# Optimization experiments

Hardware: AMD Instinct MI355X
Metric: run time of the kernel (lower is better)

## Reference

```python
import jax, jax.numpy as jnp
import numpy as np
import math

D_MODEL = 1024
N_HEAD = 16
HEAD_DIM = D_MODEL // N_HEAD
BATCH = 4
MAX_LEN = 1024


def _shift(BD):
    # BD: (b, h, L, 2L) -> (b, h, L, L), Transformer-XL relative shift
    b, h, L, _ = BD.shape
    zero_pad = jnp.zeros((b, h, L, 1), BD.dtype)
    BD = jnp.concatenate([BD, zero_pad], axis=-1)      # (b,h,L,2L+1)
    BD = BD.reshape(b, h, -1, L)[:, :, :-1]            # (b,h,2L,L)
    BD = BD.reshape(b, h, L, -1)                       # (b,h,L,2L)
    return BD[:, :, :, L:]                             # (b,h,L,L)


def setup_inputs() -> dict:
    key = jax.random.key(0)
    ks = jax.random.split(key, 10)
    s = 1.0 / math.sqrt(D_MODEL)
    return {
        "q": jax.random.normal(ks[0], (BATCH, MAX_LEN, D_MODEL), jnp.float32),
        "k": jax.random.normal(ks[1], (BATCH, MAX_LEN, D_MODEL), jnp.float32),
        "mask": jax.random.randint(ks[2], (BATCH, MAX_LEN), 0, 2, jnp.int32),
        "pos_embed": jax.random.normal(ks[3], (2 * MAX_LEN, HEAD_DIM), jnp.float32),
        "Wq": jax.random.normal(ks[4], (D_MODEL, D_MODEL), jnp.float32) * s,
        "Wkv": jax.random.normal(ks[5], (D_MODEL, 2 * D_MODEL), jnp.float32) * s,
        "Wr": jax.random.normal(ks[6], (HEAD_DIM, HEAD_DIM), jnp.float32) / math.sqrt(HEAD_DIM),
        "r_r_bias": jax.random.normal(ks[7], (N_HEAD, HEAD_DIM), jnp.float32) * 0.02,
        "r_w_bias": jax.random.normal(ks[8], (N_HEAD, HEAD_DIM), jnp.float32) * 0.02,
    }


def reference(q, k, mask, pos_embed, Wq, Wkv, Wr, r_r_bias, r_w_bias):
    B, L, D = q.shape
    H = r_r_bias.shape[0]
    hd = D // H
    scale = math.sqrt(hd)

    r = pos_embed @ Wr                                   # (2L, hd)
    qh = (q @ Wq).reshape(B, L, H, hd).transpose(0, 2, 1, 3)   # (B,H,L,hd)
    kv = k @ Wkv                                         # (B,L,2D)
    kk, vv = jnp.split(kv, 2, axis=-1)
    kh = kk.reshape(B, L, H, hd).transpose(0, 2, 1, 3)
    vh = vv.reshape(B, L, H, hd).transpose(0, 2, 1, 3)

    AC = jnp.einsum('bhqd,bhkd->bhqk', qh + r_r_bias[None, :, None, :], kh)
    BD = jnp.einsum('bhqd,ld->bhql', qh + r_w_bias[None, :, None, :], r)  # (B,H,L,2L)
    BD = _shift(BD)

    attn = (AC + BD) / scale
    attn = jnp.where(mask[:, None, None, :] == 0, -jnp.inf, attn)
    attn = jax.nn.softmax(attn, axis=-1)

    out = jnp.einsum('bhqk,bhkd->bhqd', attn, vh)        # (B,H,L,hd)
    return out.transpose(0, 2, 1, 3).reshape(B, L, D)
```

## Files before the change

kernel.cpp:

```cpp
#include <hip/hip_runtime.h>

typedef short bf16x8 __attribute__((ext_vector_type(8)));
typedef float f32x4 __attribute__((ext_vector_type(4)));
typedef unsigned short u16;
typedef unsigned short u16x4 __attribute__((ext_vector_type(4)));
typedef unsigned short u16x8 __attribute__((ext_vector_type(8)));
typedef unsigned int u32;

#define NB 4
#define LEN 1024
#define DM 1024
#define NH 16
#define HD 64

#define QSCALE 0.18033688011112043f

__device__ __forceinline__ u16 f2bf(float f) {
    union { float f; unsigned u; } v; v.f = f;
    return (u16)((v.u + 0x7fffu + ((v.u >> 16) & 1u)) >> 16);
}

__device__ __forceinline__ float bf2f(u16 x) {
    union { float f; unsigned u; } v; v.u = ((unsigned)x) << 16;
    return v.f;
}

__device__ __forceinline__ float exp2f_fast(float x) {
    float r; asm("v_exp_f32 %0, %1" : "=v"(r) : "v"(x)); return r;
}

__device__ __forceinline__ unsigned cvt_pk_bf16(float a, float b) {
    unsigned r; asm("v_cvt_pk_bf16_f32 %0, %1, %2" : "=v"(r) : "v"(a), "v"(b)); return r;
}

__device__ __forceinline__ f32x4 mfma16(bf16x8 a, bf16x8 b, f32x4 c) {
    return __builtin_amdgcn_mfma_f32_16x16x32_bf16(a, b, c, 0, 0, 0);
}

__device__ __forceinline__ void gload16(const void* g, void* l) {
    __builtin_amdgcn_global_load_lds(
        (const __attribute__((address_space(1))) unsigned int*)g,
        (__attribute__((address_space(3))) unsigned int*)l, 16, 0, 0);
}

__global__ void prep(const float* __restrict__ q, const float* __restrict__ k,
                     const int* __restrict__ msk,
                     const float* __restrict__ Wq, const float* __restrict__ Wkv,
                     const float* __restrict__ pos, const float* __restrict__ Wr,
                     u16* __restrict__ qbf, u16* __restrict__ kbf,
                     u16* __restrict__ WqT, u16* __restrict__ WkvT,
                     u16* __restrict__ rbf, float* __restrict__ mb) {
    __shared__ float tile[32][33];
    const int f = blockIdx.x;
    const int tid = threadIdx.x;
    if (f < 3072) {
        const int x = f % 96, y = f / 96;
        const bool isQ = x < 32;
        const float* W = isQ ? Wq : Wkv;
        u16* WT = isQ ? WqT : WkvT;
        const int N = isQ ? 1024 : 2048;
        const int n0 = (isQ ? x : x - 32) * 32;
        const int k0 = y * 32;
        const int tx = tid & 31, ty = tid >> 5;
        #pragma unroll
        for (int j = 0; j < 4; j++) {
            int r = ty + j * 8;
            tile[r][tx] = W[(size_t)(k0 + r) * N + n0 + tx];
        }
        __syncthreads();
        #pragma unroll
        for (int j = 0; j < 4; j++) {
            int r = ty + j * 8;
            WT[(size_t)(n0 + r) * 1024 + k0 + tx] = f2bf(tile[tx][r]);
        }
    } else if (f < 3588) {
        int idx = (f - 3072) * 256 + tid;
        if (idx < 2064 * 64) {
            int row = idx >> 6, col = idx & 63;
            float s = 0.f;
            if (row < 2048) {
                #pragma unroll
                for (int kk = 0; kk < 64; kk++) s += pos[row * 64 + kk] * Wr[kk * 64 + col];
            }
            const int csw = (((col >> 3) ^ (row & 7)) << 3) | (col & 7);
            rbf[(row << 6) | csw] = f2bf(s);
        }
    } else if (f < 3604) {
        int i = (f - 3588) * 256 + tid;
        if (i < NB * LEN) mb[i] = msk[i] ? 0.f : -3.0e38f;
    } else {
        int idx = (f - 3604) * 256 + tid;
        if (idx < 1048576) {
            float4 v = ((const float4*)q)[idx];
            u16x4 o;
            o[0] = f2bf(v.x); o[1] = f2bf(v.y); o[2] = f2bf(v.z); o[3] = f2bf(v.w);
            ((u16x4*)qbf)[idx] = o;
        } else if (idx < 2097152) {
            int i = idx - 1048576;
            float4 v = ((const float4*)k)[i];
            u16x4 o;
            o[0] = f2bf(v.x); o[1] = f2bf(v.y); o[2] = f2bf(v.z); o[3] = f2bf(v.w);
            ((u16x4*)kbf)[i] = o;
        }
    }
}

__global__ __launch_bounds__(256) void gemm_all(
    const u16* __restrict__ qbf, const u16* __restrict__ kbf,
    const u16* __restrict__ WqT, const u16* __restrict__ WkvT,
    const float* __restrict__ rrb,
    u16* __restrict__ A1,
    u16* __restrict__ khs, u16* __restrict__ vhsT)
{
    __shared__ u16 as[2][128][32];
    __shared__ u16 bs[2][128][32];

    const int fb = blockIdx.x;
    const int wsw = ((fb & 7) * 96) + (fb >> 3);
    const int bx = wsw % 24;
    const bool isQ = bx < 8;
    const u16* Abf = isQ ? qbf : kbf;
    const u16* BT  = isQ ? WqT : WkvT;
    const int n0 = (isQ ? bx : bx - 8) * 128;
    const int m0 = (wsw / 24) * 128;
    const int tid = threadIdx.x;
    const int w = tid >> 6, lane = tid & 63, g = lane >> 4, c = lane & 15;
    const int wm = w >> 1, wn = w & 1;
    const int srow = lane >> 2, sj = lane & 3;

    const f32x4 fzero = {0.f, 0.f, 0.f, 0.f};
    f32x4 acc[4][4];
    #pragma unroll
    for (int i = 0; i < 4; i++)
        #pragma unroll
        for (int j = 0; j < 4; j++) acc[i][j] = fzero;

    auto STAGE = [&](int buf, int ks) {
        const int k0 = ks * 32;
        #pragma unroll
        for (int i = 0; i < 2; i++) {
            const int rb = w * 32 + i * 16;
            const int rowA = rb + srow;
            gload16(Abf + (size_t)(m0 + rowA) * 1024 + k0 + ((sj ^ (rowA & 3)) << 3),
                    &as[buf][rb][0]);
            gload16(BT + (size_t)(n0 + rowA) * 1024 + k0 + ((sj ^ (rowA & 3)) << 3),
                    &bs[buf][rb][0]);
        }
    };

    STAGE(0, 0);
    __syncthreads();

    for (int ks = 0; ks < 32; ks++) {
        const int cur = ks & 1, nb = cur ^ 1;
        if (ks < 31) STAGE(nb, ks + 1);

        bf16x8 af[4], bfr[4];
        #pragma unroll
        for (int i = 0; i < 4; i++) {
            const int row = wm * 64 + i * 16 + c;
            af[i] = *(const bf16x8*)&as[cur][row][(g ^ (row & 3)) << 3];
        }
        #pragma unroll
        for (int j = 0; j < 4; j++) {
            const int row = wn * 64 + j * 16 + c;
            bfr[j] = *(const bf16x8*)&bs[cur][row][(g ^ (row & 3)) << 3];
        }
        #pragma unroll
        for (int i = 0; i < 4; i++)
            #pragma unroll
            for (int j = 0; j < 4; j++)
                acc[i][j] = mfma16(af[i], bfr[j], acc[i][j]);

        __syncthreads();
    }

    #pragma unroll
    for (int j = 0; j < 4; j++) {
        const int n = n0 + wn * 64 + j * 16 + c;
        float b1v = 0.f;
        if (isQ) b1v = rrb[n];
        #pragma unroll
        for (int i = 0; i < 4; i++) {
            const int l0 = m0 + wm * 64 + i * 16 + 4 * g;
            if (!isQ && n >= DM) {
                const int d = n & 63, hh = (n - DM) >> 6;
                const int bb = l0 >> 10, l = l0 & 1023;
                u16x4 o;
                #pragma unroll
                for (int r = 0; r < 4; r++) o[r] = f2bf(acc[i][j][r]);
                *(u16x4*)(vhsT + (((size_t)(bb * NH + hh)) * HD + d) * LEN + l) = o;
            } else {
                #pragma unroll
                for (int r = 0; r < 4; r++) {
                    const int row = l0 + r;
                    const int bb = row >> 10, l = row & 1023;
                    const float v = acc[i][j][r];
                    if (isQ) {
                        size_t idx = (((size_t)(bb * NH + (n >> 6))) * LEN + l) * HD + (n & 63);
                        A1[idx] = f2bf((v + b1v) * QSCALE);
                    } else {
                        const int d = n & 63;
                        const int dsw = (((d >> 3) ^ (l & 7)) << 3) | (d & 7);
                        size_t idx = (((size_t)(bb * NH + (n >> 6))) * LEN + l) * HD + dsw;
                        khs[idx] = f2bf(v);
                    }
                }
            }
        }
    }
}

__global__ __launch_bounds__(512, 4) void attn_kernel(
    const u16* __restrict__ A1,
    const u16* __restrict__ khs, const u16* __restrict__ vhsT,
    const u16* __restrict__ rbf, const float* __restrict__ mbias,
    const float* __restrict__ rrb, const float* __restrict__ rwb,
    float* __restrict__ outp)
{
    __shared__ u16 kbuf[2][32][64];
    __shared__ u16 rbuf[224][64];
    __shared__ u16 vbuf[2][4][64][8];
    __shared__ float biasl[1024];
    __shared__ float gl[8][16][52];

    const int bh = blockIdx.x;
    const int b = bh >> 4, h = bh & 15;
    const int tid = threadIdx.x;
    const int w = tid >> 6, lane = tid & 63, g = lane >> 4, c = lane & 15;
    const int q0 = blockIdx.y * 128, q0w = q0 + w * 16;
    const int lrow8 = lane >> 3, lcol = lane & 7;
    const int kkey = (c + 1) & 7;

    const u16* Kbase = khs + (size_t)bh * LEN * HD;
    const u16* Vp = vhsT + (size_t)bh * HD * LEN;
    float* glw = &gl[w][0][0];
    u16* pw = (u16*)glw;

    const u16* A1p = A1 + ((size_t)bh * LEN + q0w) * HD;
    bf16x8 a1f[2], a2f[2];
    #pragma unroll
    for (int kf = 0; kf < 2; kf++)
        a1f[kf] = *(const bf16x8*)(A1p + c * HD + kf * 32 + g * 8);
    {
        const float* rrbp = rrb + h * HD;
        const float* rwbp = rwb + h * HD;
        #pragma unroll
        for (int kf = 0; kf < 2; kf++) {
            const int dbase = kf * 32 + g * 8;
            f32x4 rA0 = *(const f32x4*)(rrbp + dbase);
            f32x4 rA1 = *(const f32x4*)(rrbp + dbase + 4);
            f32x4 rB0 = *(const f32x4*)(rwbp + dbase);
            f32x4 rB1 = *(const f32x4*)(rwbp + dbase + 4);
            float a2v[8];
            #pragma unroll
            for (int e = 0; e < 4; e++) {
                a2v[e]     = bf2f((u16)a1f[kf][e])     + (rB0[e] - rA0[e]) * QSCALE;
                a2v[4 + e] = bf2f((u16)a1f[kf][4 + e]) + (rB1[e] - rA1[e]) * QSCALE;
            }
            union { u32 u[4]; bf16x8 v; } cv;
            cv.u[0] = cvt_pk_bf16(a2v[0], a2v[1]);
            cv.u[1] = cvt_pk_bf16(a2v[2], a2v[3]);
            cv.u[2] = cvt_pk_bf16(a2v[4], a2v[5]);
            cv.u[3] = cvt_pk_bf16(a2v[6], a2v[7]);
            a2f[kf] = cv.v;
        }
    }

    const int js0 = LEN - q0 - 128;
    if (w < 4) {
        gload16(Kbase + (((size_t)(8 * w + lrow8)) << 6) + (lcol << 3), &kbuf[0][8 * w][0]);
        gload16(Vp + ((size_t)lane << 10) + 8 * w, &vbuf[0][w][0][0]);
    } else {
        gload16(mbias + b * LEN + (w - 4) * 256 + lane * 4, &biasl[(w - 4) * 256]);
    }
    #pragma unroll
    for (int i = 0; i < 3; i++) {
        const int row = js0 + 8 * (w + 8 * i);
        gload16(rbf + (((size_t)(row + lrow8)) << 6) + (lcol << 3), &rbuf[row % 224][0]);
    }
    __syncthreads();

    bf16x8 RA[2], RB[2];
    int bs = (1009 - q0w) % 224;
    {
        int t = bs + c; if (t >= 224) t -= 224;
        #pragma unroll
        for (int kf = 0; kf < 2; kf++)
            RA[kf] = *(const bf16x8*)&rbuf[t][((4 * kf + g) ^ kkey) * 8];
    }

    const f32x4 fzero = {0.f, 0.f, 0.f, 0.f};
    f32x4 oacc[4];
    #pragma unroll
    for (int dt = 0; dt < 4; dt++) oacc[dt] = fzero;
    float mrow = -3.0e38f, lrow = 0.f;

    auto STEP = [&](int kt, bf16x8 (&Rold)[2], bf16x8 (&Rnew)[2]) {
        const int cur = kt & 1, nb = cur ^ 1;
        const int c0 = kt * 32;

        if (w < 4) {
            if (kt < 31) {
                const int c0n = c0 + 32;
                gload16(Kbase + (((size_t)(c0n + 8 * w + lrow8)) << 6) + (lcol << 3), &kbuf[nb][8 * w][0]);
                gload16(Vp + ((size_t)lane << 10) + c0n + 8 * w, &vbuf[nb][w][0][0]);
            }
        } else {
            if (kt < 30) {
                const int row0 = js0 + 192 + 32 * kt + 8 * (w - 4);
                gload16(rbf + (((size_t)(row0 + lrow8)) << 6) + (lcol << 3), &rbuf[row0 % 224][0]);
            }
        }

        bf16x8 Kf[2][2];
        #pragma unroll
        for (int ct = 0; ct < 2; ct++)
            #pragma unroll
            for (int kf = 0; kf < 2; kf++)
                Kf[ct][kf] = *(const bf16x8*)&kbuf[cur][16 * ct + c][((4 * kf + g) ^ (c & 7)) * 8];

        bf16x8 Rf1[2], Rf2[2];
        {
            int t = bs + 16 + c; if (t >= 224) t -= 224;
            #pragma unroll
            for (int kf = 0; kf < 2; kf++)
                Rf1[kf] = *(const bf16x8*)&rbuf[t][((4 * kf + g) ^ kkey) * 8];
        }
        {
            int t = bs + 32 + c; if (t >= 224) t -= 224;
            #pragma unroll
            for (int kf = 0; kf < 2; kf++) {
                Rf2[kf] = *(const bf16x8*)&rbuf[t][((4 * kf + g) ^ kkey) * 8];
                Rnew[kf] = Rf2[kf];
            }
        }

        __builtin_amdgcn_s_setprio(1);
        f32x4 s0 = fzero, s1 = fzero;
        s0 = mfma16(Kf[0][0], a1f[0], s0);
        s0 = mfma16(Kf[0][1], a1f[1], s0);
        s1 = mfma16(Kf[1][0], a1f[0], s1);
        s1 = mfma16(Kf[1][1], a1f[1], s1);
        f32x4 g0 = fzero, g1 = fzero, g2 = fzero;
        g0 = mfma16(Rold[0], a2f[0], g0);
        g0 = mfma16(Rold[1], a2f[1], g0);
        *(f32x4*)&glw[c * 52 + 4 * g] = g0;
        g1 = mfma16(Rf1[0], a2f[0], g1);
        g1 = mfma16(Rf1[1], a2f[1], g1);
        *(f32x4*)&glw[c * 52 + 16 + 4 * g] = g1;
        g2 = mfma16(Rf2[0], a2f[0], g2);
        g2 = mfma16(Rf2[1], a2f[1], g2);
        *(f32x4*)&glw[c * 52 + 32 + 4 * g] = g2;
        __builtin_amdgcn_s_setprio(0);

        const float* glq = &glw[c * 52];
        f32x4 bb0 = *(const f32x4*)&biasl[c0 + 4 * g];
        f32x4 bb1 = *(const f32x4*)&biasl[c0 + 16 + 4 * g];
        #pragma unroll
        for (int r = 0; r < 4; r++) {
            const int gidx = 4 * g + r + 15 - c;
            s0[r] += glq[gidx] + bb0[r];
            s1[r] += glq[gidx + 16] + bb1[r];
        }

        float t = fmaxf(fmaxf(fmaxf(s0[0], s0[1]), fmaxf(s0[2], s0[3])),
                        fmaxf(fmaxf(s1[0], s1[1]), fmaxf(s1[2], s1[3])));
        t = fmaxf(t, __shfl_xor(t, 16));
        t = fmaxf(t, __shfl_xor(t, 32));
        if (!__all(t <= mrow + 8.f)) {
            const float mnew = fmaxf(mrow, t);
            const float alpha = exp2f_fast(mrow - mnew);
            mrow = mnew;
            lrow *= alpha;
            #pragma unroll
            for (int dt = 0; dt < 4; dt++)
                #pragma unroll
                for (int r = 0; r < 4; r++) oacc[dt][r] *= alpha;
        }
        float p[8];
        float ps = 0.f;
        #pragma unroll
        for (int r = 0; r < 4; r++) {
            p[r] = exp2f_fast(s0[r] - mrow);
            p[4 + r] = exp2f_fast(s1[r] - mrow);
            ps += p[r] + p[4 + r];
        }
        lrow += ps;
        const unsigned d0 = cvt_pk_bf16(p[0], p[1]);
        const unsigned d1 = cvt_pk_bf16(p[2], p[3]);
        const unsigned d2 = cvt_pk_bf16(p[4], p[5]);
        const unsigned d3 = cvt_pk_bf16(p[6], p[7]);
        *(uint2*)&pw[c * 104 + 4 * g] = make_uint2(d0, d1);
        *(uint2*)&pw[c * 104 + 16 + 4 * g] = make_uint2(d2, d3);
        bf16x8 pbr = *(const bf16x8*)&pw[c * 104 + 8 * g];

        bf16x8 Vb[4];
        #pragma unroll
        for (int dt = 0; dt < 4; dt++)
            Vb[dt] = *(const bf16x8*)&vbuf[cur][g][16 * dt + c][0];
        __builtin_amdgcn_s_setprio(1);
        #pragma unroll
        for (int dt = 0; dt < 4; dt++)
            oacc[dt] = mfma16(Vb[dt], pbr, oacc[dt]);
        __builtin_amdgcn_s_setprio(0);

        bs += 32; if (bs >= 224) bs -= 224;
        __syncthreads();
    };

    for (int kt2 = 0; kt2 < 16; kt2++) {
        STEP(2 * kt2,     RA, RB);
        STEP(2 * kt2 + 1, RB, RA);
    }

    float sum = lrow;
    sum += __shfl_xor(sum, 16);
    sum += __shfl_xor(sum, 32);
    const float inv = sum > 0.f ? 1.0f / sum : 0.f;
    const int l = q0w + c;
    float* op = outp + ((size_t)b * LEN + l) * DM + h * HD;
    #pragma unroll
    for (int dt = 0; dt < 4; dt++) {
        f32x4 o;
        #pragma unroll
        for (int r = 0; r < 4; r++) o[r] = oacc[dt][r] * inv;
        *(f32x4*)(op + dt * 16 + 4 * g) = o;
    }
}

extern "C" void kernel_launch(void* const* d_in, const int* in_sizes, int n_in,
                              void* d_out, int out_size, void* d_ws, size_t ws_size,
                              hipStream_t stream) {
    const float* q   = (const float*)d_in[0];
    const float* k   = (const float*)d_in[1];
    const int*   msk = (const int*)d_in[2];
    const float* pos = (const float*)d_in[3];
    const float* Wq  = (const float*)d_in[4];
    const float* Wkv = (const float*)d_in[5];
    const float* Wr  = (const float*)d_in[6];
    const float* rrb = (const float*)d_in[7];
    const float* rwb = (const float*)d_in[8];
    float* outp = (float*)d_out;
    char* ws = (char*)d_ws;

    u16* qbf  = (u16*)(ws + 0);
    u16* kbf  = (u16*)(ws + 8388608);
    u16* WqT  = (u16*)(ws + 16777216);
    u16* WkvT = (u16*)(ws + 18874368);
    u16* rbf  = (u16*)(ws + 23068672);
    u16* A1   = (u16*)(ws + 23332864);
    u16* khs  = (u16*)(ws + 40110080);
    u16* vhsT = (u16*)(ws + 48498688);
    float* mb = (float*)(ws + 56887296);

    prep<<<11796, 256, 0, stream>>>(q, k, msk, Wq, Wkv, pos, Wr, qbf, kbf, WqT, WkvT, rbf, mb);
    gemm_all<<<768, 256, 0, stream>>>(qbf, kbf, WqT, WkvT, rrb, A1, khs, vhsT);
    attn_kernel<<<dim3(64, 8), 512, 0, stream>>>(A1, khs, vhsT, rbf, mb, rrb, rwb, outp);
}
```

Before: 113.6 us.

## Fuse fp32-to-bf16 activation conversion into GEMM A-tile staging

The separate pass that converted q and k from fp32 to bf16 in a workspace is removed. The GEMM now loads fp32 A tiles into registers, converts them with packed bf16 conversions, and writes them to swizzled LDS, overlapping the load with the MFMA loop. The small pos@Wr and mask-bias jobs move from the prep kernel into extra blocks of the GEMM launch. This saves a full read-write round trip of the activations, at the cost of twice the A-tile global traffic in the GEMM, more register pressure, and one conversion per k-step per GEMM block, repeated across the 24 N tiles.

```diff
diff --git a/kernel.cpp b/kernel.cpp
--- a/kernel.cpp
+++ b/kernel.cpp
@@ -6,6 +6,7 @@
 typedef unsigned short u16x4 __attribute__((ext_vector_type(4)));
 typedef unsigned short u16x8 __attribute__((ext_vector_type(8)));
 typedef unsigned int u32;
+typedef unsigned int u32x4 __attribute__((ext_vector_type(4)));
 
 #define NB 4
 #define LEN 1024
@@ -43,90 +44,79 @@
         (__attribute__((address_space(3))) unsigned int*)l, 16, 0, 0);
 }
 
-__global__ void prep(const float* __restrict__ q, const float* __restrict__ k,
-                     const int* __restrict__ msk,
-                     const float* __restrict__ Wq, const float* __restrict__ Wkv,
-                     const float* __restrict__ pos, const float* __restrict__ Wr,
-                     u16* __restrict__ qbf, u16* __restrict__ kbf,
-                     u16* __restrict__ WqT, u16* __restrict__ WkvT,
-                     u16* __restrict__ rbf, float* __restrict__ mb) {
+__global__ void prep(const float* __restrict__ Wq, const float* __restrict__ Wkv,
+                     u16* __restrict__ WqT, u16* __restrict__ WkvT) {
     __shared__ float tile[32][33];
     const int f = blockIdx.x;
     const int tid = threadIdx.x;
-    if (f < 3072) {
-        const int x = f % 96, y = f / 96;
-        const bool isQ = x < 32;
-        const float* W = isQ ? Wq : Wkv;
-        u16* WT = isQ ? WqT : WkvT;
-        const int N = isQ ? 1024 : 2048;
-        const int n0 = (isQ ? x : x - 32) * 32;
-        const int k0 = y * 32;
-        const int tx = tid & 31, ty = tid >> 5;
-        #pragma unroll
-        for (int j = 0; j < 4; j++) {
-            int r = ty + j * 8;
-            tile[r][tx] = W[(size_t)(k0 + r) * N + n0 + tx];
-        }
-        __syncthreads();
-        #pragma unroll
-        for (int j = 0; j < 4; j++) {
-            int r = ty + j * 8;
-            WT[(size_t)(n0 + r) * 1024 + k0 + tx] = f2bf(tile[tx][r]);
-        }
-    } else if (f < 3588) {
-        int idx = (f - 3072) * 256 + tid;
-        if (idx < 2064 * 64) {
-            int row = idx >> 6, col = idx & 63;
-            float s = 0.f;
-            if (row < 2048) {
-                #pragma unroll
-                for (int kk = 0; kk < 64; kk++) s += pos[row * 64 + kk] * Wr[kk * 64 + col];
-            }
-            const int csw = (((col >> 3) ^ (row & 7)) << 3) | (col & 7);
-            rbf[(row << 6) | csw] = f2bf(s);
-        }
-    } else if (f < 3604) {
-        int i = (f - 3588) * 256 + tid;
-        if (i < NB * LEN) mb[i] = msk[i] ? 0.f : -3.0e38f;
-    } else {
-        int idx = (f - 3604) * 256 + tid;
-        if (idx < 1048576) {
-            float4 v = ((const float4*)q)[idx];
-            u16x4 o;
-            o[0] = f2bf(v.x); o[1] = f2bf(v.y); o[2] = f2bf(v.z); o[3] = f2bf(v.w);
-            ((u16x4*)qbf)[idx] = o;
-        } else if (idx < 2097152) {
-            int i = idx - 1048576;
-            float4 v = ((const float4*)k)[i];
-            u16x4 o;
-            o[0] = f2bf(v.x); o[1] = f2bf(v.y); o[2] = f2bf(v.z); o[3] = f2bf(v.w);
-            ((u16x4*)kbf)[i] = o;
-        }
+    const int x = f % 96, y = f / 96;
+    const bool isQ = x < 32;
+    const float* W = isQ ? Wq : Wkv;
+    u16* WT = isQ ? WqT : WkvT;
+    const int N = isQ ? 1024 : 2048;
+    const int n0 = (isQ ? x : x - 32) * 32;
+    const int k0 = y * 32;
+    const int tx = tid & 31, ty = tid >> 5;
+    #pragma unroll
+    for (int j = 0; j < 4; j++) {
+        int r = ty + j * 8;
+        tile[r][tx] = W[(size_t)(k0 + r) * N + n0 + tx];
+    }
+    __syncthreads();
+    #pragma unroll
+    for (int j = 0; j < 4; j++) {
+        int r = ty + j * 8;
+        WT[(size_t)(n0 + r) * 1024 + k0 + tx] = f2bf(tile[tx][r]);
     }
 }
 
 __global__ __launch_bounds__(256) void gemm_all(
-    const u16* __restrict__ qbf, const u16* __restrict__ kbf,
+    const float* __restrict__ qf, const float* __restrict__ kf32,
     const u16* __restrict__ WqT, const u16* __restrict__ WkvT,
     const float* __restrict__ rrb,
+    const float* __restrict__ pos, const float* __restrict__ Wr,
+    const int* __restrict__ msk,
     u16* __restrict__ A1,
-    u16* __restrict__ khs, u16* __restrict__ vhsT)
+    u16* __restrict__ khs, u16* __restrict__ vhsT,
+    u16* __restrict__ rbf, float* __restrict__ mb)
 {
     __shared__ u16 as[2][128][32];
     __shared__ u16 bs[2][128][32];
 
     const int fb = blockIdx.x;
+    const int tid = threadIdx.x;
+
+    if (fb >= 768) {
+        if (fb < 1284) {
+            int idx = (fb - 768) * 256 + tid;
+            if (idx < 2064 * 64) {
+                int row = idx >> 6, col = idx & 63;
+                float s = 0.f;
+                if (row < 2048) {
+                    #pragma unroll
+                    for (int kk = 0; kk < 64; kk++) s += pos[row * 64 + kk] * Wr[kk * 64 + col];
+                }
+                const int csw = (((col >> 3) ^ (row & 7)) << 3) | (col & 7);
+                rbf[(row << 6) | csw] = f2bf(s);
+            }
+        } else {
+            int i = (fb - 1284) * 256 + tid;
+            if (i < NB * LEN) mb[i] = msk[i] ? 0.f : -3.0e38f;
+        }
+        return;
+    }
+
     const int wsw = ((fb & 7) * 96) + (fb >> 3);
     const int bx = wsw % 24;
     const bool isQ = bx < 8;
-    const u16* Abf = isQ ? qbf : kbf;
+    const float* Af = isQ ? qf : kf32;
     const u16* BT  = isQ ? WqT : WkvT;
     const int n0 = (isQ ? bx : bx - 8) * 128;
     const int m0 = (wsw / 24) * 128;
-    const int tid = threadIdx.x;
     const int w = tid >> 6, lane = tid & 63, g = lane >> 4, c = lane & 15;
     const int wm = w >> 1, wn = w & 1;
     const int srow = lane >> 2, sj = lane & 3;
+    const int arow = tid >> 1, ahalf = tid & 1;
 
     const f32x4 fzero = {0.f, 0.f, 0.f, 0.f};
     f32x4 acc[4][4];
@@ -135,25 +125,40 @@
         #pragma unroll
         for (int j = 0; j < 4; j++) acc[i][j] = fzero;
 
-    auto STAGE = [&](int buf, int ks) {
+    float4 fa[4];
+    const float* Abase = Af + (size_t)(m0 + arow) * 1024 + ahalf * 16;
+
+    auto STAGE_LOAD = [&](int ks, int buf) {
         const int k0 = ks * 32;
+        const float4* Ap = (const float4*)(Abase + k0);
+        fa[0] = Ap[0]; fa[1] = Ap[1]; fa[2] = Ap[2]; fa[3] = Ap[3];
         #pragma unroll
         for (int i = 0; i < 2; i++) {
             const int rb = w * 32 + i * 16;
-            const int rowA = rb + srow;
-            gload16(Abf + (size_t)(m0 + rowA) * 1024 + k0 + ((sj ^ (rowA & 3)) << 3),
-                    &as[buf][rb][0]);
-            gload16(BT + (size_t)(n0 + rowA) * 1024 + k0 + ((sj ^ (rowA & 3)) << 3),
+            const int rowB = rb + srow;
+            gload16(BT + (size_t)(n0 + rowB) * 1024 + k0 + ((sj ^ (rowB & 3)) << 3),
                     &bs[buf][rb][0]);
         }
     };
 
-    STAGE(0, 0);
+    auto STAGE_WRITE = [&](int buf) {
+        u32x4 d0, d1;
+        d0[0] = cvt_pk_bf16(fa[0].x, fa[0].y); d0[1] = cvt_pk_bf16(fa[0].z, fa[0].w);
+        d0[2] = cvt_pk_bf16(fa[1].x, fa[1].y); d0[3] = cvt_pk_bf16(fa[1].z, fa[1].w);
+        d1[0] = cvt_pk_bf16(fa[2].x, fa[2].y); d1[1] = cvt_pk_bf16(fa[2].z, fa[2].w);
+        d1[2] = cvt_pk_bf16(fa[3].x, fa[3].y); d1[3] = cvt_pk_bf16(fa[3].z, fa[3].w);
+        const int j0 = 2 * ahalf, j1 = j0 + 1;
+        *(u32x4*)&as[buf][arow][((j0 ^ (arow & 3)) << 3)] = d0;
+        *(u32x4*)&as[buf][arow][((j1 ^ (arow & 3)) << 3)] = d1;
+    };
+
+    STAGE_LOAD(0, 0);
+    STAGE_WRITE(0);
     __syncthreads();
 
     for (int ks = 0; ks < 32; ks++) {
         const int cur = ks & 1, nb = cur ^ 1;
-        if (ks < 31) STAGE(nb, ks + 1);
+        if (ks < 31) STAGE_LOAD(ks + 1, nb);
 
         bf16x8 af[4], bfr[4];
         #pragma unroll
@@ -172,6 +177,7 @@
             for (int j = 0; j < 4; j++)
                 acc[i][j] = mfma16(af[i], bfr[j], acc[i][j]);
 
+        if (ks < 31) STAGE_WRITE(nb);
         __syncthreads();
     }
 
@@ -444,8 +450,6 @@
     float* outp = (float*)d_out;
     char* ws = (char*)d_ws;
 
-    u16* qbf  = (u16*)(ws + 0);
-    u16* kbf  = (u16*)(ws + 8388608);
     u16* WqT  = (u16*)(ws + 16777216);
     u16* WkvT = (u16*)(ws + 18874368);
     u16* rbf  = (u16*)(ws + 23068672);
@@ -454,7 +458,8 @@
     u16* vhsT = (u16*)(ws + 48498688);
     float* mb = (float*)(ws + 56887296);
 
-    prep<<<11796, 256, 0, stream>>>(q, k, msk, Wq, Wkv, pos, Wr, qbf, kbf, WqT, WkvT, rbf, mb);
-    gemm_all<<<768, 256, 0, stream>>>(qbf, kbf, WqT, WkvT, rrb, A1, khs, vhsT);
+    prep<<<3072, 256, 0, stream>>>(Wq, Wkv, WqT, WkvT);
+    gemm_all<<<1300, 256, 0, stream>>>(q, k, WqT, WkvT, rrb, pos, Wr, msk,
+                                       A1, khs, vhsT, rbf, mb);
     attn_kernel<<<dim3(64, 8), 512, 0, stream>>>(A1, khs, vhsT, rbf, mb, rrb, rwb, outp);
 }
```

Measured after the change: 138.5 us. 1.22x slower.
